# Performance work log

Measured on AMD Instinct MI355X. Metric: run time of the kernel, lower is better.

## Reference

```python
import jax, jax.numpy as jnp
import numpy as np

N = 100000   # nodes
E = 1600000  # edges
G = 64       # graphs in batch
C = 8        # num_classes
H = 128      # hidden dim


def _lin(k, out_f, in_f):
    return jax.random.normal(k, (out_f, in_f), jnp.float32) * (1.0 / np.sqrt(in_f))


def setup_inputs() -> dict:
    key = jax.random.key(0)
    ks = jax.random.split(key, 16)
    x = jax.random.normal(ks[0], (N, 5), jnp.float32)
    edge_index = jax.random.randint(ks[1], (2, E), 0, N)
    batch = jnp.sort(jax.random.randint(ks[2], (N,), 0, G))
    exinfo = jax.random.normal(ks[3], (G, 10), jnp.float32)
    return {
        "x": x, "edge_index": edge_index, "batch": batch, "exinfo": exinfo,
        # GraphConv1: 3 -> 128 (PyG GraphConv: lin_root(x) + lin_rel(scatter_add(x_j)))
        "Wroot1": _lin(ks[4], H, 3), "Wrel1": _lin(ks[5], H, 3), "brel1": jnp.zeros((H,), jnp.float32),
        # GraphConv2: 128 -> 128
        "Wroot2": _lin(ks[6], H, H), "Wrel2": _lin(ks[7], H, H), "brel2": jnp.zeros((H,), jnp.float32),
        # MLP head
        "W1": _lin(ks[8], 64, 2 * H + 10), "b1": jnp.zeros((64,), jnp.float32),
        "W2": _lin(ks[9], 32, 64), "b2": jnp.zeros((32,), jnp.float32),
        "W3": _lin(ks[10], C, 32), "b3": jnp.zeros((C,), jnp.float32),
    }


def _graph_conv(x, src, dst, Wroot, Wrel, brel):
    # PyG GraphConv (aggr='add'): out_i = Wrel @ sum_{j->i} x_j + brel + Wroot @ x_i
    agg = jax.ops.segment_sum(x[src], dst, num_segments=x.shape[0])  # [N, F]
    return agg @ Wrel.T + brel + x @ Wroot.T


def reference(x, edge_index, batch, exinfo,
              Wroot1, Wrel1, brel1, Wroot2, Wrel2, brel2,
              W1, b1, W2, b2, W3, b3):
    xs = x[:, 2:5]                              # data.x[:, 2:5]
    src, dst = edge_index[0], edge_index[1]
    x1 = jax.nn.relu(_graph_conv(xs, src, dst, Wroot1, Wrel1, brel1))   # [N, 128]
    x2 = jax.nn.relu(_graph_conv(x1, src, dst, Wroot2, Wrel2, brel2))   # [N, 128]
    h = jnp.concatenate([x1, x2], axis=-1)      # [N, 256]
    g = jax.ops.segment_max(h, batch, num_segments=G)  # global max pool [G, 256]
    g = jnp.concatenate([g, exinfo], axis=-1)   # [G, 266]
    g = jax.nn.relu(g @ W1.T + b1)
    g = jax.nn.relu(g @ W2.T + b2)
    return jax.nn.log_softmax(g @ W3.T + b3, axis=-1)
```

## Files before the change

### kernel.cpp

```cpp
#include <hip/hip_runtime.h>

#define N_NODES 100000
#define N_EDGES 1600000
#define NG 64
#define NC 8
#define HD 128

#define BUCKET_SHIFT 8
#define NB ((N_NODES + 255) >> 8)
#define NCHUNK 256
#define EPC (N_EDGES / NCHUNK)

typedef __attribute__((ext_vector_type(8))) __bf16 bf16x8;
typedef __attribute__((ext_vector_type(4))) float f32x4;


__global__ void bin_hist_k(const int* __restrict__ dst, int* __restrict__ hist) {
  __shared__ int lh[NB];
  int c = blockIdx.x, t = threadIdx.x;
  for (int b = t; b < NB; b += 256) lh[b] = 0;
  __syncthreads();
  int e0 = c * EPC;
  for (int i = t; i < EPC; i += 256) atomicAdd(&lh[dst[e0 + i] >> BUCKET_SHIFT], 1);
  __syncthreads();
  for (int b = t; b < NB; b += 256) hist[c * NB + b] = lh[b];
}

__launch_bounds__(512)
__global__ void base_k(const int* __restrict__ hist, int* __restrict__ bucket_base,
                       int* __restrict__ row_ptr) {
  __shared__ int tot[512];
  int t = threadIdx.x;
  int s = 0;
  if (t < NB)
    for (int c = 0; c < NCHUNK; c++) s += hist[c * NB + t];
  tot[t] = s;
  __syncthreads();
  for (int off = 1; off < 512; off <<= 1) {
    int v = (t >= off) ? tot[t - off] : 0;
    __syncthreads();
    tot[t] += v;
    __syncthreads();
  }
  if (t < NB) bucket_base[t] = tot[t] - s;
  if (t == 0) { bucket_base[NB] = N_EDGES; row_ptr[N_NODES] = N_EDGES; }
}

__global__ void chunk_scan_k(int* __restrict__ hist, const int* __restrict__ bucket_base) {
  int b = blockIdx.x, lane = threadIdx.x;
  int carry = bucket_base[b];
#pragma unroll
  for (int it = 0; it < NCHUNK / 64; it++) {
    int c = it * 64 + lane;
    int v = hist[c * NB + b];
    int s = v;
#pragma unroll
    for (int off = 1; off < 64; off <<= 1) {
      int u = __shfl_up(s, off);
      if (lane >= off) s += u;
    }
    hist[c * NB + b] = carry + s - v;
    carry += __shfl(s, 63);
  }
}

__global__ void scatter_k(const int* __restrict__ src, const int* __restrict__ dst,
                          const int* __restrict__ hist, int2* __restrict__ pairs) {
  __shared__ int loff[NB];
  int c = blockIdx.x, t = threadIdx.x;
  for (int b = t; b < NB; b += 256) loff[b] = hist[c * NB + b];
  __syncthreads();
  int e0 = c * EPC;
  for (int i = t; i < EPC; i += 256) {
    int d = dst[e0 + i], s = src[e0 + i];
    int pos = atomicAdd(&loff[d >> BUCKET_SHIFT], 1);
    pairs[pos] = make_int2(d, s);
  }
}

__global__ void bucket_csr_k(const int2* __restrict__ pairs,
                             const int* __restrict__ bucket_base,
                             int* __restrict__ row_ptr, int* __restrict__ csr) {
  __shared__ int cnt[256];
  __shared__ int start[256];
  __shared__ int wsum[4];
  int b = blockIdx.x, t = threadIdx.x, lane = t & 63, wid = t >> 6;
  int nb0 = b << BUCKET_SHIFT;
  int beg = bucket_base[b], end = bucket_base[b + 1];
  cnt[t] = 0;
  __syncthreads();
  for (int i = beg + t; i < end; i += 256) atomicAdd(&cnt[pairs[i].x - nb0], 1);
  __syncthreads();
  int v = cnt[t];
  int s = v;
#pragma unroll
  for (int off = 1; off < 64; off <<= 1) {
    int u = __shfl_up(s, off);
    if (lane >= off) s += u;
  }
  if (lane == 63) wsum[wid] = s;
  __syncthreads();
  if (t == 0) {
    int a = 0;
    for (int j = 0; j < 4; j++) { int x = wsum[j]; wsum[j] = a; a += x; }
  }
  __syncthreads();
  int excl = wsum[wid] + s - v;
  start[t] = excl;
  if (nb0 + t < N_NODES) row_ptr[nb0 + t] = beg + excl;
  cnt[t] = 0;
  __syncthreads();
  for (int i = beg + t; i < end; i += 256) {
    int2 p = pairs[i];
    int li = p.x - nb0;
    int pos = beg + start[li] + atomicAdd(&cnt[li], 1);
    csr[pos] = p.y;
  }
}


__global__ void conv1_k(const float* __restrict__ x, const int* __restrict__ row_ptr,
                        const int* __restrict__ csr, const float* __restrict__ Wroot1,
                        const float* __restrict__ Wrel1, const float* __restrict__ brel1,
                        __bf16* __restrict__ xcat) {
  int node = blockIdx.x * 4 + (threadIdx.x >> 6);
  if (node >= N_NODES) return;
  int lane = threadIdx.x & 63;
  int beg = row_ptr[node], end = row_ptr[node + 1];
  float a0 = 0.f, a1 = 0.f, a2 = 0.f;
  for (int e = beg + lane; e < end; e += 64) {
    int s = csr[e];
    const float* xp = x + (size_t)s * 5;
    a0 += xp[2]; a1 += xp[3]; a2 += xp[4];
  }
#pragma unroll
  for (int m = 1; m < 64; m <<= 1) {
    a0 += __shfl_xor(a0, m);
    a1 += __shfl_xor(a1, m);
    a2 += __shfl_xor(a2, m);
  }
  const float* xn = x + (size_t)node * 5;
  float r0 = xn[2], r1 = xn[3], r2 = xn[4];
  __bf16* orow = xcat + (size_t)node * 256 + 128;
#pragma unroll
  for (int hh = 0; hh < 2; hh++) {
    int h = lane + hh * 64;
    float v = brel1[h]
            + a0 * Wrel1[h * 3 + 0] + a1 * Wrel1[h * 3 + 1] + a2 * Wrel1[h * 3 + 2]
            + r0 * Wroot1[h * 3 + 0] + r1 * Wroot1[h * 3 + 1] + r2 * Wroot1[h * 3 + 2];
    orow[h] = (__bf16)fmaxf(v, 0.f);
  }
}


#define LDROW(s) (*((const uint4*)(xcat + (size_t)(s) * 256 + 128) + f))
#define ACC8(u) \
  acc[0] += __uint_as_float((u).x << 16);  acc[1] += __uint_as_float((u).x & 0xffff0000u); \
  acc[2] += __uint_as_float((u).y << 16);  acc[3] += __uint_as_float((u).y & 0xffff0000u); \
  acc[4] += __uint_as_float((u).z << 16);  acc[5] += __uint_as_float((u).z & 0xffff0000u); \
  acc[6] += __uint_as_float((u).w << 16);  acc[7] += __uint_as_float((u).w & 0xffff0000u);

__global__ void agg2_k(const int* __restrict__ row_ptr, const int* __restrict__ csr,
                       __bf16* xcat) {
  int node = blockIdx.x * 4 + (threadIdx.x >> 6);
  if (node >= N_NODES) return;
  int lane = threadIdx.x & 63;
  int g = lane >> 4, f = lane & 15;
  int beg = row_ptr[node], end = row_ptr[node + 1];
  int deg = end - beg;
  int idx = (lane < deg) ? csr[beg + lane] : 0;
  float acc[8];
#pragma unroll
  for (int k = 0; k < 8; k++) acc[k] = 0.f;
  int dmain = deg < 64 ? deg : 64;
  int j = 0;
  for (; j + 16 <= dmain; j += 16) {
    int s0 = __shfl(idx, j + g);
    int s1 = __shfl(idx, j + 4 + g);
    int s2 = __shfl(idx, j + 8 + g);
    int s3 = __shfl(idx, j + 12 + g);
    uint4 u0 = LDROW(s0);
    uint4 u1 = LDROW(s1);
    uint4 u2 = LDROW(s2);
    uint4 u3 = LDROW(s3);
    ACC8(u0) ACC8(u1) ACC8(u2) ACC8(u3)
  }
  if (j + 8 <= dmain) {
    int s0 = __shfl(idx, j + g);
    int s1 = __shfl(idx, j + 4 + g);
    uint4 u0 = LDROW(s0);
    uint4 u1 = LDROW(s1);
    ACC8(u0) ACC8(u1)
    j += 8;
  }
  if (j + 4 <= dmain) {
    int s0 = __shfl(idx, j + g);
    uint4 u0 = LDROW(s0);
    ACC8(u0)
    j += 4;
  }
  {
    int rem = dmain - j;
    int s0 = __shfl(idx, j + (g < rem ? g : 0));
    if (g < rem) {
      uint4 u0 = LDROW(s0);
      ACC8(u0)
    }
  }
  for (int e = beg + 64; e < end; e += 4) {
    int m = end - e;
    int s0 = csr[e + (g < m ? g : 0)];
    if (g < m) {
      uint4 u0 = LDROW(s0);
      ACC8(u0)
    }
  }
#pragma unroll
  for (int k = 0; k < 8; k++) {
    acc[k] += __shfl_xor(acc[k], 16);
    acc[k] += __shfl_xor(acc[k], 32);
  }
  if (g == 0) {
    uint4 o;
    o.x = (__float_as_uint((float)(__bf16)acc[0]) >> 16) | (__float_as_uint((float)(__bf16)acc[1]) & 0xffff0000u);
    o.y = (__float_as_uint((float)(__bf16)acc[2]) >> 16) | (__float_as_uint((float)(__bf16)acc[3]) & 0xffff0000u);
    o.z = (__float_as_uint((float)(__bf16)acc[4]) >> 16) | (__float_as_uint((float)(__bf16)acc[5]) & 0xffff0000u);
    o.w = (__float_as_uint((float)(__bf16)acc[6]) >> 16) | (__float_as_uint((float)(__bf16)acc[7]) & 0xffff0000u);
    *((uint4*)(xcat + (size_t)node * 256) + f) = o;
  }
}


__global__ void build_wc_k(const float* __restrict__ Wrel2, const float* __restrict__ Wroot2,
                           __bf16* __restrict__ Wc) {
  int i = blockIdx.x * 256 + threadIdx.x;
  int h = i >> 8, k = i & 255;
  float v = (k < 128) ? Wrel2[h * 128 + k] : Wroot2[h * 128 + (k - 128)];
  Wc[i] = (__bf16)v;
}


__launch_bounds__(512, 4)
__global__ void gemm2_k(const __bf16* __restrict__ xcat, const __bf16* __restrict__ Wc,
                        const float* __restrict__ brel2, const int* __restrict__ batch,
                        unsigned int* __restrict__ gout) {
  __shared__ char Blds[128 * 256 * 2];
  int t = threadIdx.x;
  for (int i = t; i < 4096; i += 512) {
    uint4 v = ((const uint4*)Wc)[i];
    int byte = i * 16;
    int sw = byte ^ (((byte >> 9) & 7) << 4);
    *(uint4*)(Blds + sw) = v;
  }
  __syncthreads();
  int wid = t >> 6, lane = t & 63;
  int nb = (blockIdx.x * 8 + wid) * 32;
  if (nb >= N_NODES) return;
  int r = lane & 15, ko = lane >> 4;
  const __bf16* arow0 = xcat + (size_t)(nb + r) * 256 + ko * 8;
  const __bf16* arow1 = arow0 + 16 * 256;
  f32x4 acc0[8], acc1[8];
#pragma unroll
  for (int i = 0; i < 8; i++) {
    acc0[i] = (f32x4){0.f, 0.f, 0.f, 0.f};
    acc1[i] = (f32x4){0.f, 0.f, 0.f, 0.f};
  }
#pragma unroll
  for (int kb = 0; kb < 256; kb += 32) {
    bf16x8 a0 = *(const bf16x8*)(arow0 + kb);
    bf16x8 a1 = *(const bf16x8*)(arow1 + kb);
#pragma unroll
    for (int ht = 0; ht < 8; ht++) {
      int h = ht * 16 + r;
      int byte = h * 512 + ko * 16 + kb * 2;
      bf16x8 b = *(const bf16x8*)(Blds + (byte ^ ((r & 7) << 4)));
      acc0[ht] = __builtin_amdgcn_mfma_f32_16x16x32_bf16(a0, b, acc0[ht], 0, 0, 0);
      acc1[ht] = __builtin_amdgcn_mfma_f32_16x16x32_bf16(a1, b, acc1[ht], 0, 0, 0);
    }
  }
  int gfirst = batch[nb], glast = batch[nb + 31];
  if (gfirst == glast) {
    unsigned int* gp = gout + gfirst * 256 + 128;
#pragma unroll
    for (int ht = 0; ht < 8; ht++) {
      float bias = brel2[ht * 16 + r];
      float m = 0.f;
#pragma unroll
      for (int rr = 0; rr < 4; rr++) {
        m = fmaxf(m, acc0[ht][rr] + bias);
        m = fmaxf(m, acc1[ht][rr] + bias);
      }
      m = fmaxf(m, __shfl_xor(m, 16));
      m = fmaxf(m, __shfl_xor(m, 32));
      if (ko == 0) atomicMax(&gp[ht * 16 + r], __float_as_uint(m));
    }
  } else {
    int g0[4], g1[4];
#pragma unroll
    for (int rr = 0; rr < 4; rr++) {
      g0[rr] = batch[nb + ko * 4 + rr];
      g1[rr] = batch[nb + 16 + ko * 4 + rr];
    }
#pragma unroll
    for (int ht = 0; ht < 8; ht++) {
      int h = ht * 16 + r;
      float bias = brel2[h];
#pragma unroll
      for (int rr = 0; rr < 4; rr++) {
        atomicMax(&gout[g0[rr] * 256 + 128 + h],
                  __float_as_uint(fmaxf(acc0[ht][rr] + bias, 0.f)));
        atomicMax(&gout[g1[rr] * 256 + 128 + h],
                  __float_as_uint(fmaxf(acc1[ht][rr] + bias, 0.f)));
      }
    }
  }
}


__global__ void segmax1_k(const __bf16* __restrict__ xcat, const int* __restrict__ batch,
                          unsigned int* __restrict__ g) {
  int t = threadIdx.x;
  int f = t & 63;
  int s = t >> 6;
  int n0 = blockIdx.x * 256;
  float m0 = 0.f, m1 = 0.f;
  int cur = -1;
  int n1 = n0 + 256 < N_NODES ? n0 + 256 : N_NODES;
  for (int n = n0 + s; n < n1; n += 4) {
    int b = batch[n];
    if (b != cur) {
      if (cur >= 0) {
        atomicMax(&g[cur * 256 + 2 * f], __float_as_uint(m0));
        atomicMax(&g[cur * 256 + 2 * f + 1], __float_as_uint(m1));
      }
      cur = b; m0 = 0.f; m1 = 0.f;
    }
    unsigned int u = ((const unsigned int*)(xcat + (size_t)n * 256 + 128))[f];
    m0 = fmaxf(m0, __uint_as_float(u << 16));
    m1 = fmaxf(m1, __uint_as_float(u & 0xffff0000u));
  }
  if (cur >= 0) {
    atomicMax(&g[cur * 256 + 2 * f], __float_as_uint(m0));
    atomicMax(&g[cur * 256 + 2 * f + 1], __float_as_uint(m1));
  }
}


__global__ void head1_k(const float* __restrict__ g, const float* __restrict__ exinfo,
                        const float* __restrict__ W1, const float* __restrict__ b1,
                        float* __restrict__ g1) {
  int gg = blockIdx.x;
  int t = threadIdx.x;
  int c = t >> 2, q = t & 3;
  const float* w = W1 + c * 266;
  const float* gr = g + gg * 256;
  float s = 0.f;
  for (int k = q * 64; k < q * 64 + 64; k++) s += gr[k] * w[k];
  if (q == 0) {
    const float* er = exinfo + gg * 10;
    for (int k = 0; k < 10; k++) s += er[k] * w[256 + k];
    s += b1[c];
  }
  s += __shfl_xor(s, 1);
  s += __shfl_xor(s, 2);
  if (q == 0) g1[gg * 64 + c] = fmaxf(s, 0.f);
}

__global__ void head2_k(const float* __restrict__ g1, const float* __restrict__ W2,
                        const float* __restrict__ b2, const float* __restrict__ W3,
                        const float* __restrict__ b3, float* __restrict__ out) {
  __shared__ float s1[64 * 64];
  __shared__ float s2[64 * 32];
  int t = threadIdx.x;
  for (int i = t; i < 4096; i += 256) s1[i] = g1[i];
  __syncthreads();
  for (int o = t; o < 2048; o += 256) {
    int r = o >> 5, c = o & 31;
    float s = b2[c];
    for (int k = 0; k < 64; k++) s += s1[r * 64 + k] * W2[c * 64 + k];
    s2[r * 32 + c] = fmaxf(s, 0.f);
  }
  __syncthreads();
  if (t < 64) {
    float lg[8];
#pragma unroll
    for (int c = 0; c < 8; c++) {
      float s = b3[c];
      for (int k = 0; k < 32; k++) s += s2[t * 32 + k] * W3[c * 32 + k];
      lg[c] = s;
    }
    float mx = lg[0];
#pragma unroll
    for (int c = 1; c < 8; c++) mx = fmaxf(mx, lg[c]);
    float se = 0.f;
#pragma unroll
    for (int c = 0; c < 8; c++) se += expf(lg[c] - mx);
    float lse = mx + logf(se);
#pragma unroll
    for (int c = 0; c < 8; c++) out[t * 8 + c] = lg[c] - lse;
  }
}


extern "C" void kernel_launch(void* const* d_in, const int* in_sizes, int n_in,
                              void* d_out, int out_size, void* d_ws, size_t ws_size,
                              hipStream_t stream) {
  const float* x      = (const float*)d_in[0];
  const int*   edge   = (const int*)d_in[1];
  const int*   batch  = (const int*)d_in[2];
  const float* exinfo = (const float*)d_in[3];
  const float* Wroot1 = (const float*)d_in[4];
  const float* Wrel1  = (const float*)d_in[5];
  const float* brel1  = (const float*)d_in[6];
  const float* Wroot2 = (const float*)d_in[7];
  const float* Wrel2  = (const float*)d_in[8];
  const float* brel2  = (const float*)d_in[9];
  const float* W1     = (const float*)d_in[10];
  const float* b1     = (const float*)d_in[11];
  const float* W2     = (const float*)d_in[12];
  const float* b2     = (const float*)d_in[13];
  const float* W3     = (const float*)d_in[14];
  const float* b3     = (const float*)d_in[15];
  const int* src = edge;
  const int* dst = edge + N_EDGES;

  char* p = (char*)d_ws;
  auto alloc = [&](size_t bytes) {
    char* q = p;
    p += (bytes + 511) & ~(size_t)511;
    return (void*)q;
  };
  __bf16*       Wc          = (__bf16*)alloc(128 * 256 * 2);
  unsigned int* g           = (unsigned int*)alloc(64 * 256 * 4);
  float*        g1          = (float*)alloc(64 * 64 * 4);
  int*          hist        = (int*)alloc((size_t)NCHUNK * NB * 4);
  int*          bucket_base = (int*)alloc((size_t)(NB + 1) * 4);
  int*          row_ptr     = (int*)alloc((size_t)(N_NODES + 1) * 4);
  int*          csr         = (int*)alloc((size_t)N_EDGES * 4);
  __bf16*       xcat        = (__bf16*)alloc((size_t)N_NODES * 256 * 2);
  int2*         pairs       = (int2*)alloc((size_t)N_EDGES * 8);

  hipMemsetAsync(g, 0, 64 * 256 * 4, stream);
  build_wc_k<<<128, 256, 0, stream>>>(Wrel2, Wroot2, Wc);
  bin_hist_k<<<NCHUNK, 256, 0, stream>>>(dst, hist);
  base_k<<<1, 512, 0, stream>>>(hist, bucket_base, row_ptr);
  chunk_scan_k<<<NB, 64, 0, stream>>>(hist, bucket_base);
  scatter_k<<<NCHUNK, 256, 0, stream>>>(src, dst, hist, pairs);
  bucket_csr_k<<<NB, 256, 0, stream>>>(pairs, bucket_base, row_ptr, csr);
  conv1_k<<<25000, 256, 0, stream>>>(x, row_ptr, csr, Wroot1, Wrel1, brel1, xcat);
  agg2_k<<<25000, 256, 0, stream>>>(row_ptr, csr, xcat);
  gemm2_k<<<391, 512, 0, stream>>>(xcat, Wc, brel2, batch, g);
  segmax1_k<<<NB, 256, 0, stream>>>(xcat, batch, g);
  head1_k<<<64, 256, 0, stream>>>((const float*)g, exinfo, W1, b1, g1);
  head2_k<<<1, 256, 0, stream>>>(g1, W2, b2, W3, b3, (float*)d_out);
}
```

Measured before the change: 213.7 us.

## Pack edge pairs into 32-bit words, pad node features, use packed float2 accumulation

Edge pairs are now stored as a single 32-bit word: the source index shifted left by 8, with the low 8 bits holding the destination's offset within its bucket. This halves the pairs buffer traffic between the scatter and CSR kernels. A new pre-pass copies the 3 used feature columns into padded float4 rows, so conv1 gathers each neighbour with one 16-byte load instead of three strided loads. agg2 now accumulates into float2 vectors so the compiler can emit packed FP32 adds. The costs are an extra kernel launch, an extra 1.6 MB buffer, and a packing scheme that only works while node indices fit in 24 bits.

```diff
diff --git a/kernel.cpp b/kernel.cpp
--- a/kernel.cpp
+++ b/kernel.cpp
@@ -13,6 +13,7 @@
 
 typedef __attribute__((ext_vector_type(8))) __bf16 bf16x8;
 typedef __attribute__((ext_vector_type(4))) float f32x4;
+typedef __attribute__((ext_vector_type(2))) float f32x2;
 
 
 __global__ void bin_hist_k(const int* __restrict__ dst, int* __restrict__ hist) {
@@ -65,7 +66,7 @@
 }
 
 __global__ void scatter_k(const int* __restrict__ src, const int* __restrict__ dst,
-                          const int* __restrict__ hist, int2* __restrict__ pairs) {
+                          const int* __restrict__ hist, unsigned int* __restrict__ pairs) {
   __shared__ int loff[NB];
   int c = blockIdx.x, t = threadIdx.x;
   for (int b = t; b < NB; b += 256) loff[b] = hist[c * NB + b];
@@ -74,11 +75,11 @@
   for (int i = t; i < EPC; i += 256) {
     int d = dst[e0 + i], s = src[e0 + i];
     int pos = atomicAdd(&loff[d >> BUCKET_SHIFT], 1);
-    pairs[pos] = make_int2(d, s);
-  }
-}
-
-__global__ void bucket_csr_k(const int2* __restrict__ pairs,
+    pairs[pos] = ((unsigned int)s << 8) | (unsigned int)(d & 255);
+  }
+}
+
+__global__ void bucket_csr_k(const unsigned int* __restrict__ pairs,
                              const int* __restrict__ bucket_base,
                              int* __restrict__ row_ptr, int* __restrict__ csr) {
   __shared__ int cnt[256];
@@ -89,7 +90,7 @@
   int beg = bucket_base[b], end = bucket_base[b + 1];
   cnt[t] = 0;
   __syncthreads();
-  for (int i = beg + t; i < end; i += 256) atomicAdd(&cnt[pairs[i].x - nb0], 1);
+  for (int i = beg + t; i < end; i += 256) atomicAdd(&cnt[pairs[i] & 255u], 1);
   __syncthreads();
   int v = cnt[t];
   int s = v;
@@ -111,15 +112,24 @@
   cnt[t] = 0;
   __syncthreads();
   for (int i = beg + t; i < end; i += 256) {
-    int2 p = pairs[i];
-    int li = p.x - nb0;
+    unsigned int p = pairs[i];
+    int li = p & 255u;
     int pos = beg + start[li] + atomicAdd(&cnt[li], 1);
-    csr[pos] = p.y;
-  }
-}
-
-
-__global__ void conv1_k(const float* __restrict__ x, const int* __restrict__ row_ptr,
+    csr[pos] = (int)(p >> 8);
+  }
+}
+
+
+__global__ void pack_xs_k(const float* __restrict__ x, float4* __restrict__ xs4) {
+  int i = blockIdx.x * 256 + threadIdx.x;
+  if (i < N_NODES) {
+    const float* xp = x + (size_t)i * 5;
+    xs4[i] = make_float4(xp[2], xp[3], xp[4], 0.f);
+  }
+}
+
+
+__global__ void conv1_k(const float4* __restrict__ xs4, const int* __restrict__ row_ptr,
                         const int* __restrict__ csr, const float* __restrict__ Wroot1,
                         const float* __restrict__ Wrel1, const float* __restrict__ brel1,
                         __bf16* __restrict__ xcat) {
@@ -129,9 +139,8 @@
   int beg = row_ptr[node], end = row_ptr[node + 1];
   float a0 = 0.f, a1 = 0.f, a2 = 0.f;
   for (int e = beg + lane; e < end; e += 64) {
-    int s = csr[e];
-    const float* xp = x + (size_t)s * 5;
-    a0 += xp[2]; a1 += xp[3]; a2 += xp[4];
+    float4 v = xs4[csr[e]];
+    a0 += v.x; a1 += v.y; a2 += v.z;
   }
 #pragma unroll
   for (int m = 1; m < 64; m <<= 1) {
@@ -139,15 +148,14 @@
     a1 += __shfl_xor(a1, m);
     a2 += __shfl_xor(a2, m);
   }
-  const float* xn = x + (size_t)node * 5;
-  float r0 = xn[2], r1 = xn[3], r2 = xn[4];
+  float4 rv = xs4[node];
   __bf16* orow = xcat + (size_t)node * 256 + 128;
 #pragma unroll
   for (int hh = 0; hh < 2; hh++) {
     int h = lane + hh * 64;
     float v = brel1[h]
             + a0 * Wrel1[h * 3 + 0] + a1 * Wrel1[h * 3 + 1] + a2 * Wrel1[h * 3 + 2]
-            + r0 * Wroot1[h * 3 + 0] + r1 * Wroot1[h * 3 + 1] + r2 * Wroot1[h * 3 + 2];
+            + rv.x * Wroot1[h * 3 + 0] + rv.y * Wroot1[h * 3 + 1] + rv.z * Wroot1[h * 3 + 2];
     orow[h] = (__bf16)fmaxf(v, 0.f);
   }
 }
@@ -155,10 +163,10 @@
 
 #define LDROW(s) (*((const uint4*)(xcat + (size_t)(s) * 256 + 128) + f))
 #define ACC8(u) \
-  acc[0] += __uint_as_float((u).x << 16);  acc[1] += __uint_as_float((u).x & 0xffff0000u); \
-  acc[2] += __uint_as_float((u).y << 16);  acc[3] += __uint_as_float((u).y & 0xffff0000u); \
-  acc[4] += __uint_as_float((u).z << 16);  acc[5] += __uint_as_float((u).z & 0xffff0000u); \
-  acc[6] += __uint_as_float((u).w << 16);  acc[7] += __uint_as_float((u).w & 0xffff0000u);
+  acc2[0] += (f32x2){__uint_as_float((u).x << 16), __uint_as_float((u).x & 0xffff0000u)}; \
+  acc2[1] += (f32x2){__uint_as_float((u).y << 16), __uint_as_float((u).y & 0xffff0000u)}; \
+  acc2[2] += (f32x2){__uint_as_float((u).z << 16), __uint_as_float((u).z & 0xffff0000u)}; \
+  acc2[3] += (f32x2){__uint_as_float((u).w << 16), __uint_as_float((u).w & 0xffff0000u)};
 
 __global__ void agg2_k(const int* __restrict__ row_ptr, const int* __restrict__ csr,
                        __bf16* xcat) {
@@ -169,9 +177,9 @@
   int beg = row_ptr[node], end = row_ptr[node + 1];
   int deg = end - beg;
   int idx = (lane < deg) ? csr[beg + lane] : 0;
-  float acc[8];
-#pragma unroll
-  for (int k = 0; k < 8; k++) acc[k] = 0.f;
+  f32x2 acc2[4];
+#pragma unroll
+  for (int k = 0; k < 4; k++) acc2[k] = (f32x2){0.f, 0.f};
   int dmain = deg < 64 ? deg : 64;
   int j = 0;
   for (; j + 16 <= dmain; j += 16) {
@@ -216,16 +224,18 @@
     }
   }
 #pragma unroll
-  for (int k = 0; k < 8; k++) {
-    acc[k] += __shfl_xor(acc[k], 16);
-    acc[k] += __shfl_xor(acc[k], 32);
+  for (int k = 0; k < 4; k++) {
+    acc2[k].x += __shfl_xor(acc2[k].x, 16);
+    acc2[k].y += __shfl_xor(acc2[k].y, 16);
+    acc2[k].x += __shfl_xor(acc2[k].x, 32);
+    acc2[k].y += __shfl_xor(acc2[k].y, 32);
   }
   if (g == 0) {
     uint4 o;
-    o.x = (__float_as_uint((float)(__bf16)acc[0]) >> 16) | (__float_as_uint((float)(__bf16)acc[1]) & 0xffff0000u);
-    o.y = (__float_as_uint((float)(__bf16)acc[2]) >> 16) | (__float_as_uint((float)(__bf16)acc[3]) & 0xffff0000u);
-    o.z = (__float_as_uint((float)(__bf16)acc[4]) >> 16) | (__float_as_uint((float)(__bf16)acc[5]) & 0xffff0000u);
-    o.w = (__float_as_uint((float)(__bf16)acc[6]) >> 16) | (__float_as_uint((float)(__bf16)acc[7]) & 0xffff0000u);
+    o.x = (__float_as_uint((float)(__bf16)acc2[0].x) >> 16) | (__float_as_uint((float)(__bf16)acc2[0].y) & 0xffff0000u);
+    o.y = (__float_as_uint((float)(__bf16)acc2[1].x) >> 16) | (__float_as_uint((float)(__bf16)acc2[1].y) & 0xffff0000u);
+    o.z = (__float_as_uint((float)(__bf16)acc2[2].x) >> 16) | (__float_as_uint((float)(__bf16)acc2[2].y) & 0xffff0000u);
+    o.w = (__float_as_uint((float)(__bf16)acc2[3].x) >> 16) | (__float_as_uint((float)(__bf16)acc2[3].y) & 0xffff0000u);
     *((uint4*)(xcat + (size_t)node * 256) + f) = o;
   }
 }
@@ -433,21 +443,23 @@
   __bf16*       Wc          = (__bf16*)alloc(128 * 256 * 2);
   unsigned int* g           = (unsigned int*)alloc(64 * 256 * 4);
   float*        g1          = (float*)alloc(64 * 64 * 4);
+  float4*       xs4         = (float4*)alloc((size_t)N_NODES * 16);
   int*          hist        = (int*)alloc((size_t)NCHUNK * NB * 4);
   int*          bucket_base = (int*)alloc((size_t)(NB + 1) * 4);
   int*          row_ptr     = (int*)alloc((size_t)(N_NODES + 1) * 4);
   int*          csr         = (int*)alloc((size_t)N_EDGES * 4);
   __bf16*       xcat        = (__bf16*)alloc((size_t)N_NODES * 256 * 2);
-  int2*         pairs       = (int2*)alloc((size_t)N_EDGES * 8);
+  unsigned int* pairs       = (unsigned int*)alloc((size_t)N_EDGES * 4);
 
   hipMemsetAsync(g, 0, 64 * 256 * 4, stream);
   build_wc_k<<<128, 256, 0, stream>>>(Wrel2, Wroot2, Wc);
+  pack_xs_k<<<NB, 256, 0, stream>>>(x, xs4);
   bin_hist_k<<<NCHUNK, 256, 0, stream>>>(dst, hist);
   base_k<<<1, 512, 0, stream>>>(hist, bucket_base, row_ptr);
   chunk_scan_k<<<NB, 64, 0, stream>>>(hist, bucket_base);
   scatter_k<<<NCHUNK, 256, 0, stream>>>(src, dst, hist, pairs);
   bucket_csr_k<<<NB, 256, 0, stream>>>(pairs, bucket_base, row_ptr, csr);
-  conv1_k<<<25000, 256, 0, stream>>>(x, row_ptr, csr, Wroot1, Wrel1, brel1, xcat);
+  conv1_k<<<25000, 256, 0, stream>>>(xs4, row_ptr, csr, Wroot1, Wrel1, brel1, xcat);
   agg2_k<<<25000, 256, 0, stream>>>(row_ptr, csr, xcat);
   gemm2_k<<<391, 512, 0, stream>>>(xcat, Wc, brel2, batch, g);
   segmax1_k<<<NB, 256, 0, stream>>>(xcat, batch, g);
```

Result: no change. 215.4 us (+0.8%).
